# Performance work log

Measured on AMD Instinct MI355X. Metric: run time of the kernel, lower is better.

## Reference

```python
import jax, jax.numpy as jnp
import numpy as np

HIDDEN = 2048
NUM_HEADS = 16
HEAD_DIM = 128
ROPE_BASE = 10000.0
B, L = 2, 2048


def _rotate_half(x):
    x1, x2 = jnp.split(x, 2, axis=-1)
    return jnp.concatenate((-x2, x1), axis=-1)


def _apply_rope(x, position_ids, base=ROPE_BASE):
    # x: [B, L, H, D]; position_ids: [L] (broadcast over batch)
    D = x.shape[-1]
    dim_idx = jnp.arange(0, D, 2, dtype=jnp.float32)
    inv_freq = 1.0 / (base ** (dim_idx / D))                      # [D/2]
    freqs = position_ids.astype(jnp.float32)[None, :, None] * inv_freq  # [1, L, D/2]
    # NOTE: faithful to source: sin/cos are repeat_interleaved ([s0,s0,s1,s1,...])
    sin = jnp.repeat(jnp.sin(freqs), 2, axis=-1)[:, :, None, :]   # [1, L, 1, D]
    cos = jnp.repeat(jnp.cos(freqs), 2, axis=-1)[:, :, None, :]
    return cos * x + _rotate_half(x) * sin


def setup_inputs() -> dict:
    key = jax.random.key(0)
    k1, k2, k3, k4, k5 = jax.random.split(key, 5)
    hidden_states = jax.random.normal(k1, (B, L, HIDDEN), dtype=jnp.float32)
    # causal additive mask, broadcastable over heads
    causal = jnp.tril(jnp.ones((L, L), dtype=bool))
    attention_mask = jnp.where(causal, 0.0, -1e9).astype(jnp.float32)
    attention_mask = jnp.broadcast_to(attention_mask, (B, 1, L, L))
    position_ids = jnp.arange(L, dtype=jnp.int64)
    s = 1.0 / np.sqrt(HIDDEN)
    Wq = jax.random.normal(k2, (HIDDEN, NUM_HEADS * HEAD_DIM), dtype=jnp.float32) * s
    Wk = jax.random.normal(k3, (HIDDEN, NUM_HEADS * HEAD_DIM), dtype=jnp.float32) * s
    Wv = jax.random.normal(k4, (HIDDEN, NUM_HEADS * HEAD_DIM), dtype=jnp.float32) * s
    Wo = jax.random.normal(k5, (NUM_HEADS * HEAD_DIM, HIDDEN), dtype=jnp.float32) * s
    return {"hidden_states": hidden_states, "attention_mask": attention_mask,
            "position_ids": position_ids, "Wq": Wq, "Wk": Wk, "Wv": Wv, "Wo": Wo}


def reference(hidden_states, attention_mask, position_ids, Wq, Wk, Wv, Wo):
    Bb, Ll, _ = hidden_states.shape
    H, D = NUM_HEADS, HEAD_DIM
    scale = D ** -0.5
    q = (hidden_states @ Wq).reshape(Bb, Ll, H, D)
    k = (hidden_states @ Wk).reshape(Bb, Ll, H, D)
    v = (hidden_states @ Wv).reshape(Bb, Ll, H, D)
    q = _apply_rope(q, position_ids)
    k = _apply_rope(k, position_ids)
    # [B, H, Lq, Lk]
    scores = jnp.einsum('bqhd,bkhd->bhqk', q, k) * scale + attention_mask
    attn = jax.nn.softmax(scores.astype(jnp.float32), axis=-1).astype(q.dtype)
    out = jnp.einsum('bhqk,bkhd->bqhd', attn, v).reshape(Bb, Ll, H * D)
    return out @ Wo
```

## Files before the change

### kernel.cpp

```cpp
#include <hip/hip_runtime.h>
#include <stdint.h>

typedef uint16_t u16;
typedef __attribute__((ext_vector_type(4))) float f32x4;
typedef __attribute__((ext_vector_type(2))) unsigned short u16x2;
typedef __attribute__((ext_vector_type(4))) unsigned short u16x4;
typedef __attribute__((ext_vector_type(8))) __bf16 bf16x8;

#define HIDDEN 2048
#define LSEQ   2048
#define NH     16
#define HD     128
#define NQK    6144

__device__ __forceinline__ u16 f2b(float f) {
  union { float f; uint32_t u; } v; v.f = f;
  uint32_t r = v.u + 0x7fffu + ((v.u >> 16) & 1u);
  return (u16)(r >> 16);
}
__device__ __forceinline__ float b2f(u16 h) {
  union { uint32_t u; float f; } v; v.u = ((uint32_t)h) << 16;
  return v.f;
}

__device__ __forceinline__ void gload16(const void* g, void* l) {
  __builtin_amdgcn_global_load_lds((const __attribute__((address_space(1))) void*)g,
                                   (__attribute__((address_space(3))) void*)l, 16, 0, 0);
}
__device__ __forceinline__ f32x4 mfma16(bf16x8 a, bf16x8 b, f32x4 c) {
  return __builtin_amdgcn_mfma_f32_16x16x32_bf16(a, b, c, 0, 0, 0);
}

__global__ void k_f32_to_bf16(const float* __restrict__ in, u16* __restrict__ out, int n4) {
  int i = blockIdx.x * 256 + threadIdx.x;
  if (i >= n4) return;
  float4 v = ((const float4*)in)[i];
  u16x4 o = { f2b(v.x), f2b(v.y), f2b(v.z), f2b(v.w) };
  ((u16x4*)out)[i] = o;
}

__global__ __launch_bounds__(256) void k_transpose_bf16(const float* __restrict__ W,
                                                        u16* __restrict__ WT, int R, int C) {
  __shared__ u16 tile[64][65];
  const int bx = blockIdx.x, by = blockIdx.y;
  const int t = threadIdx.x;
  const int g = t >> 4, k = t & 15;
#pragma unroll
  for (int p = 0; p < 4; ++p) {
    int r = by * 64 + p * 16 + g;
    int c = bx * 64 + k * 4;
    float4 v = *(const float4*)(W + (size_t)r * C + c);
    tile[p * 16 + g][k * 4 + 0] = f2b(v.x);
    tile[p * 16 + g][k * 4 + 1] = f2b(v.y);
    tile[p * 16 + g][k * 4 + 2] = f2b(v.z);
    tile[p * 16 + g][k * 4 + 3] = f2b(v.w);
  }
  __syncthreads();
#pragma unroll
  for (int p = 0; p < 4; ++p) {
    int n = bx * 64 + p * 16 + g;
    int kk = by * 64 + k * 4;
    u16x4 o = { tile[k * 4 + 0][p * 16 + g], tile[k * 4 + 1][p * 16 + g],
                tile[k * 4 + 2][p * 16 + g], tile[k * 4 + 3][p * 16 + g] };
    *(u16x4*)(WT + (size_t)n * R + kk) = o;
  }
}

__global__ __launch_bounds__(256) void k_transpose_v(const u16* __restrict__ qkv,
                                                     u16* __restrict__ vt) {
  __shared__ u16 tile[64][65];
  const int lt = blockIdx.x;
  const int dt = blockIdx.y;
  const int bh = blockIdx.z;
  const int t = threadIdx.x;
  const int g = t >> 4, k = t & 15;
  const u16* src = qkv + (size_t)(bh >> 4) * LSEQ * NQK + 2 * HIDDEN + (bh & 15) * HD;
#pragma unroll
  for (int p = 0; p < 4; ++p) {
    int l = lt * 64 + p * 16 + g;
    int d = dt * 64 + k * 4;
    u16x4 v = *(const u16x4*)(src + (size_t)l * NQK + d);
    tile[p * 16 + g][k * 4 + 0] = v[0];
    tile[p * 16 + g][k * 4 + 1] = v[1];
    tile[p * 16 + g][k * 4 + 2] = v[2];
    tile[p * 16 + g][k * 4 + 3] = v[3];
  }
  __syncthreads();
  u16* dst = vt + (size_t)bh * HD * LSEQ;
#pragma unroll
  for (int p = 0; p < 4; ++p) {
    int d = dt * 64 + p * 16 + g;
    int l = lt * 64 + k * 4;
    u16x4 o = { tile[k * 4 + 0][p * 16 + g], tile[k * 4 + 1][p * 16 + g],
                tile[k * 4 + 2][p * 16 + g], tile[k * 4 + 3][p * 16 + g] };
    *(u16x4*)(dst + (size_t)d * LSEQ + l) = o;
  }
}

__global__ void k_rope_table(const int* __restrict__ pos, float* __restrict__ tab, int pstride) {
  int i = blockIdx.x * 256 + threadIdx.x;
  int l = i >> 6, j = i & 63;
  float p = (float)pos[(size_t)l * pstride];
  float th = p * expf(-(float)j * 0.14391156642178528f);
  tab[2 * i + 0] = cosf(th);
  tab[2 * i + 1] = sinf(th);
}

__global__ void k_rope_apply(u16* __restrict__ qkv, const float* __restrict__ tab) {
  int i = blockIdx.x * 256 + threadIdx.x;
  int dph = i & 31;
  int h = (i >> 5) & 15;
  int mat = (i >> 9) & 1;
  int row = i >> 10;
  int l = row & (LSEQ - 1);
  const float* t1 = tab + 2 * (l * 64 + dph);
  const float* t2 = tab + 2 * (l * 64 + 32 + dph);
  float s = mat ? 1.0f : 0.08838834764831845f;
  size_t base = (size_t)row * NQK + mat * HIDDEN + h * HD + dph * 2;
  u16x2 xa = *(u16x2*)(qkv + base);
  u16x2 xb = *(u16x2*)(qkv + base + 64);
  float x1a = b2f(xa[0]), x1b = b2f(xa[1]), x2a = b2f(xb[0]), x2b = b2f(xb[1]);
  u16x2 oa = { f2b((t1[0] * x1a - t1[1] * x2a) * s), f2b((t1[0] * x1b - t1[1] * x2b) * s) };
  u16x2 ob = { f2b((t2[0] * x2a + t2[1] * x1a) * s), f2b((t2[0] * x2b + t2[1] * x1b) * s) };
  *(u16x2*)(qkv + base) = oa;
  *(u16x2*)(qkv + base + 64) = ob;
}

template<int BF16OUT>
__global__ __launch_bounds__(512, 2) void k_gemm2(const u16* __restrict__ A,
                                                  const u16* __restrict__ Bt,
                                                  void* __restrict__ Cv,
                                                  int M, int N, int K) {
  __shared__ __align__(16) char lds[147456];
  const int tid = threadIdx.x, w = tid >> 6, lane = tid & 63;
  const int l15 = lane & 15, l4 = lane >> 4;
  const int wm = w >> 2, wn = w & 3;
  const int nbx = gridDim.x;
  const int nwg = nbx * gridDim.y;
  const int id = blockIdx.y * nbx + blockIdx.x;
  const int qq = nwg >> 3;
  const int sid = (id & 7) * qq + (id >> 3);
  const int bn = sid % nbx, bm = sid / nbx;
  const u16* Ag = A + (size_t)bm * 128 * K;
  const u16* Bg = Bt + (size_t)bn * 256 * K;
  const int r7 = (tid >> 3) & 7;
  const int sw0 = ((0 + l4) ^ (l15 & 7)) * 16;
  const int sw1 = ((4 + l4) ^ (l15 & 7)) * 16;

  auto stageA = [&](int kt, int buf) {
    char* dst = lds + buf * 16384;
    const int k0 = kt << 6;
#pragma unroll
    for (int i = 0; i < 2; ++i) {
      int c = i * 512 + tid;
      int row = c >> 3, s = (c & 7) ^ r7;
      gload16(Ag + (size_t)row * K + k0 + s * 8, dst + (i * 512 + w * 64) * 16);
    }
  };
  auto stageBh = [&](int kt, int buf, int half) {
    char* dst = lds + 49152 + buf * 32768;
    const int k0 = kt << 6;
#pragma unroll
    for (int i = 0; i < 2; ++i) {
      int c = half * 1024 + i * 512 + tid;
      int row = c >> 3, s = (c & 7) ^ r7;
      gload16(Bg + (size_t)row * K + k0 + s * 8, dst + (half * 1024 + i * 512 + w * 64) * 16);
    }
  };

  const int NT = K >> 6;
  stageA(0, 0); stageBh(0, 0, 0); stageBh(0, 0, 1);
  stageA(1, 1); stageBh(1, 1, 0); stageBh(1, 1, 1);
  asm volatile("s_waitcnt vmcnt(6)" ::: "memory");
  __builtin_amdgcn_s_barrier();
  asm volatile("" ::: "memory");

  f32x4 acc[4][4] = {};
  int buf = 0, sbuf = 2;
  for (int t = 0; t < NT; ++t) {
    const char* Ab = lds + buf * 16384;
    const char* Bb = lds + 49152 + buf * 32768;
    const bool doStage = (t + 2 < NT);
    bf16x8 af[4][2], bfr[4][2];
    auto rdA = [&](int mi, int ks) {
      return *(const bf16x8*)(Ab + ((wm * 64 + mi * 16 + l15) << 7) + (ks ? sw1 : sw0));
    };
    auto rdB = [&](int nj, int ks) {
      return *(const bf16x8*)(Bb + ((wn * 64 + nj * 16 + l15) << 7) + (ks ? sw1 : sw0));
    };

#pragma unroll
    for (int mi = 0; mi < 2; ++mi) { af[mi][0] = rdA(mi, 0); af[mi][1] = rdA(mi, 1); }
#pragma unroll
    for (int nj = 0; nj < 2; ++nj) { bfr[nj][0] = rdB(nj, 0); bfr[nj][1] = rdB(nj, 1); }
    if (doStage) stageA(t + 2, sbuf);
    __builtin_amdgcn_s_setprio(1);
#pragma unroll
    for (int mi = 0; mi < 2; ++mi)
#pragma unroll
      for (int nj = 0; nj < 2; ++nj) {
        acc[mi][nj] = mfma16(af[mi][0], bfr[nj][0], acc[mi][nj]);
        acc[mi][nj] = mfma16(af[mi][1], bfr[nj][1], acc[mi][nj]);
      }
    __builtin_amdgcn_s_setprio(0);

#pragma unroll
    for (int nj = 2; nj < 4; ++nj) { bfr[nj][0] = rdB(nj, 0); bfr[nj][1] = rdB(nj, 1); }
    if (doStage) stageBh(t + 2, sbuf, 0);
    __builtin_amdgcn_s_setprio(1);
#pragma unroll
    for (int mi = 0; mi < 2; ++mi)
#pragma unroll
      for (int nj = 2; nj < 4; ++nj) {
        acc[mi][nj] = mfma16(af[mi][0], bfr[nj][0], acc[mi][nj]);
        acc[mi][nj] = mfma16(af[mi][1], bfr[nj][1], acc[mi][nj]);
      }
    __builtin_amdgcn_s_setprio(0);

#pragma unroll
    for (int mi = 2; mi < 4; ++mi) { af[mi][0] = rdA(mi, 0); af[mi][1] = rdA(mi, 1); }
    if (doStage) stageBh(t + 2, sbuf, 1);
    __builtin_amdgcn_s_setprio(1);
#pragma unroll
    for (int mi = 2; mi < 4; ++mi)
#pragma unroll
      for (int nj = 2; nj < 4; ++nj) {
        acc[mi][nj] = mfma16(af[mi][0], bfr[nj][0], acc[mi][nj]);
        acc[mi][nj] = mfma16(af[mi][1], bfr[nj][1], acc[mi][nj]);
      }
    __builtin_amdgcn_s_setprio(0);

    __builtin_amdgcn_s_setprio(1);
#pragma unroll
    for (int mi = 2; mi < 4; ++mi)
#pragma unroll
      for (int nj = 0; nj < 2; ++nj) {
        acc[mi][nj] = mfma16(af[mi][0], bfr[nj][0], acc[mi][nj]);
        acc[mi][nj] = mfma16(af[mi][1], bfr[nj][1], acc[mi][nj]);
      }
    __builtin_amdgcn_s_setprio(0);

    if (doStage) asm volatile("s_waitcnt vmcnt(6)" ::: "memory");
    else         asm volatile("s_waitcnt vmcnt(0)" ::: "memory");
    __builtin_amdgcn_s_barrier();
    asm volatile("" ::: "memory");
    buf = (buf == 2) ? 0 : buf + 1;
    sbuf = (sbuf == 2) ? 0 : sbuf + 1;
  }

#pragma unroll
  for (int mi = 0; mi < 4; ++mi) {
#pragma unroll
    for (int nj = 0; nj < 4; ++nj) {
      int row0 = bm * 128 + wm * 64 + mi * 16 + l4 * 4;
      int col  = bn * 256 + wn * 64 + nj * 16 + l15;
#pragma unroll
      for (int r = 0; r < 4; ++r) {
        float v = acc[mi][nj][r];
        if (BF16OUT) ((u16*)Cv)[(size_t)(row0 + r) * N + col] = f2b(v);
        else         ((float*)Cv)[(size_t)(row0 + r) * N + col] = v;
      }
    }
  }
}

__global__ __launch_bounds__(512) void k_attn(const u16* __restrict__ qkv,
                                              const u16* __restrict__ vt,
                                              u16* __restrict__ aout) {
  __shared__ __align__(16) u16 Ks[3][64 * 128];
  __shared__ __align__(16) u16 Vs[3][128 * 64];
  __shared__ __align__(16) u16 Ps[2][8 * 16 * 72];
  const int bid = blockIdx.x;
  const int bh = bid & 31, pairi = bid >> 5;
  const int b = bh >> 4, h = bh & 15;
  const int qtA = pairi, qtB = 15 - pairi;
  const int tid = threadIdx.x, w = tid >> 6, lane = tid & 63;
  const int l15 = lane & 15, l4 = lane >> 4;

  bf16x8 qfA[4], qfB[4];
  {
    const u16* qpA = qkv + (size_t)(b * LSEQ + qtA * 128 + w * 16 + l15) * NQK + h * HD;
    const u16* qpB = qkv + (size_t)(b * LSEQ + qtB * 128 + w * 16 + l15) * NQK + h * HD;
#pragma unroll
    for (int ks = 0; ks < 4; ++ks) {
      qfA[ks] = *(const bf16x8*)(qpA + ks * 32 + l4 * 8);
      qfB[ks] = *(const bf16x8*)(qpB + ks * 32 + l4 * 8);
    }
  }

  f32x4 accA[8] = {}, accB[8] = {};
  float mA[4], lA[4], mB[4], lB[4];
#pragma unroll
  for (int r = 0; r < 4; ++r) { mA[r] = -1e30f; lA[r] = 0.f; mB[r] = -1e30f; lB[r] = 0.f; }

  const u16* kb  = qkv + (size_t)b * LSEQ * NQK + HIDDEN + h * HD;
  const u16* vtb = vt + (size_t)bh * HD * LSEQ;
  const int ntA = 2 * qtA + 2, ntB = 2 * qtB + 2;
  const int qbaseA = qtA * 128 + w * 16, qbaseB = qtB * 128 + w * 16;

  auto stage = [&](int t, int bf) {
    const int kv0 = t * 64;
    char* Kd = (char*)(&Ks[bf][0]);
    char* Vd = (char*)(&Vs[bf][0]);
#pragma unroll
    for (int p = 0; p < 2; ++p) {
      int cc = p * 512 + tid;
      int row = cc >> 4, sl = cc & 15;
      gload16(kb + (size_t)(kv0 + row) * NQK + ((sl ^ (row & 7)) * 8), Kd + (p * 512 + w * 64) * 16);
    }
#pragma unroll
    for (int p = 0; p < 2; ++p) {
      int cc = p * 512 + tid;
      int d = cc >> 3, sl = cc & 7;
      gload16(vtb + (size_t)d * LSEQ + kv0 + ((sl ^ (d & 7)) * 8), Vd + (p * 512 + w * 64) * 16);
    }
  };

  auto softmaxWrite = [&](f32x4 (&accs)[4], f32x4 (&acc_o)[8], float (&mrun)[4],
                          float (&lrun)[4], int qbase, int kv0, u16* ps) {
    const int qrow0 = qbase + l4 * 4;
    float pv[4][4], pmax[4];
    if (kv0 + 63 <= qbase) {
#pragma unroll
      for (int r = 0; r < 4; ++r) {
        pmax[r] = fmaxf(fmaxf(accs[0][r], accs[1][r]), fmaxf(accs[2][r], accs[3][r]));
#pragma unroll
        for (int nj = 0; nj < 4; ++nj) pv[nj][r] = accs[nj][r];
      }
    } else {
#pragma unroll
      for (int r = 0; r < 4; ++r) {
        float mx = -3e38f;
#pragma unroll
        for (int nj = 0; nj < 4; ++nj) {
          int kvcol = kv0 + nj * 16 + l15;
          float sv = (kvcol <= qrow0 + r) ? accs[nj][r] : -3e38f;
          pv[nj][r] = sv;
          mx = fmaxf(mx, sv);
        }
        pmax[r] = mx;
      }
    }
#pragma unroll
    for (int r = 0; r < 4; ++r) {
      pmax[r] = fmaxf(pmax[r], __shfl_xor(pmax[r], 1));
      pmax[r] = fmaxf(pmax[r], __shfl_xor(pmax[r], 2));
      pmax[r] = fmaxf(pmax[r], __shfl_xor(pmax[r], 4));
      pmax[r] = fmaxf(pmax[r], __shfl_xor(pmax[r], 8));
    }
    bool need = false;
#pragma unroll
    for (int r = 0; r < 4; ++r) need = need || (pmax[r] > mrun[r] + 8.f);
    if (__any(need)) {
#pragma unroll
      for (int r = 0; r < 4; ++r) {
        float nm = fmaxf(mrun[r], pmax[r]);
        float cf = __expf(mrun[r] - nm);
        mrun[r] = nm;
        lrun[r] *= cf;
#pragma unroll
        for (int df = 0; df < 8; ++df) acc_o[df][r] *= cf;
      }
    }
#pragma unroll
    for (int r = 0; r < 4; ++r) {
      float s = 0.f;
#pragma unroll
      for (int nj = 0; nj < 4; ++nj) {
        float e = __expf(pv[nj][r] - mrun[r]);
        pv[nj][r] = e;
        s += e;
      }
      s += __shfl_xor(s, 1);
      s += __shfl_xor(s, 2);
      s += __shfl_xor(s, 4);
      s += __shfl_xor(s, 8);
      lrun[r] += s;
    }
#pragma unroll
    for (int nj = 0; nj < 4; ++nj)
#pragma unroll
      for (int r = 0; r < 4; ++r)
        ps[(w * 16 + l4 * 4 + r) * 72 + nj * 16 + l15] = f2b(pv[nj][r]);
  };

  stage(0, 0);
  stage(1, 1);
  asm volatile("s_waitcnt vmcnt(4)" ::: "memory");
  __builtin_amdgcn_s_barrier();

  int buf = 0, sbuf = 2;
  for (int t = 0; t < ntB; ++t) {
    const bool doStage = (t + 2 < ntB);
    if (doStage) stage(t + 2, sbuf);
    const int kv0 = t * 64;
    const char* KsC = (const char*)(&Ks[buf][0]);
    const char* VsC = (const char*)(&Vs[buf][0]);
    const bool doA = (t < ntA) && (kv0 <= qbaseA + 15);
    const bool doB = (kv0 <= qbaseB + 15);

    if (doA) {
      f32x4 sA[4] = {}, sB[4] = {};
      __builtin_amdgcn_s_setprio(1);
#pragma unroll
      for (int ks = 0; ks < 4; ++ks) {
#pragma unroll
        for (int nj = 0; nj < 4; ++nj) {
          int row = nj * 16 + l15;
          int co = (ks * 64 + l4 * 16) ^ ((row & 7) << 4);
          bf16x8 kf = *(const bf16x8*)(KsC + row * 256 + co);
          sA[nj] = mfma16(qfA[ks], kf, sA[nj]);
          sB[nj] = mfma16(qfB[ks], kf, sB[nj]);
        }
      }
      __builtin_amdgcn_s_setprio(0);
      softmaxWrite(sA, accA, mA, lA, qbaseA, kv0, &Ps[0][0]);
      softmaxWrite(sB, accB, mB, lB, qbaseB, kv0, &Ps[1][0]);
      bf16x8 paA[2], paB[2];
#pragma unroll
      for (int ks2 = 0; ks2 < 2; ++ks2) {
        paA[ks2] = *(const bf16x8*)(&Ps[0][0] + (w * 16 + l15) * 72 + ks2 * 32 + l4 * 8);
        paB[ks2] = *(const bf16x8*)(&Ps[1][0] + (w * 16 + l15) * 72 + ks2 * 32 + l4 * 8);
      }
      __builtin_amdgcn_s_setprio(1);
#pragma unroll
      for (int df = 0; df < 8; ++df) {
#pragma unroll
        for (int ks2 = 0; ks2 < 2; ++ks2) {
          int vrow = df * 16 + l15;
          int co = (ks2 * 64 + l4 * 16) ^ ((vrow & 7) << 4);
          bf16x8 bv = *(const bf16x8*)(VsC + vrow * 128 + co);
          accA[df] = mfma16(paA[ks2], bv, accA[df]);
          accB[df] = mfma16(paB[ks2], bv, accB[df]);
        }
      }
      __builtin_amdgcn_s_setprio(0);
    } else if (doB) {
      f32x4 sB[4] = {};
      __builtin_amdgcn_s_setprio(1);
#pragma unroll
      for (int ks = 0; ks < 4; ++ks) {
#pragma unroll
        for (int nj = 0; nj < 4; ++nj) {
          int row = nj * 16 + l15;
          int co = (ks * 64 + l4 * 16) ^ ((row & 7) << 4);
          bf16x8 kf = *(const bf16x8*)(KsC + row * 256 + co);
          sB[nj] = mfma16(qfB[ks], kf, sB[nj]);
        }
      }
      __builtin_amdgcn_s_setprio(0);
      softmaxWrite(sB, accB, mB, lB, qbaseB, kv0, &Ps[1][0]);
      bf16x8 paB[2];
#pragma unroll
      for (int ks2 = 0; ks2 < 2; ++ks2)
        paB[ks2] = *(const bf16x8*)(&Ps[1][0] + (w * 16 + l15) * 72 + ks2 * 32 + l4 * 8);
      __builtin_amdgcn_s_setprio(1);
#pragma unroll
      for (int df = 0; df < 8; ++df) {
#pragma unroll
        for (int ks2 = 0; ks2 < 2; ++ks2) {
          int vrow = df * 16 + l15;
          int co = (ks2 * 64 + l4 * 16) ^ ((vrow & 7) << 4);
          bf16x8 bv = *(const bf16x8*)(VsC + vrow * 128 + co);
          accB[df] = mfma16(paB[ks2], bv, accB[df]);
        }
      }
      __builtin_amdgcn_s_setprio(0);
    }

    if (doStage) asm volatile("s_waitcnt vmcnt(4)" ::: "memory");
    else         asm volatile("s_waitcnt vmcnt(0)" ::: "memory");
    __builtin_amdgcn_s_barrier();
    buf = (buf == 2) ? 0 : buf + 1;
    sbuf = (sbuf == 2) ? 0 : sbuf + 1;
  }

#pragma unroll
  for (int r = 0; r < 4; ++r) {
    float invA = 1.f / lA[r];
    float invB = 1.f / lB[r];
    u16* opA = aout + (size_t)(b * LSEQ + qtA * 128 + w * 16 + l4 * 4 + r) * HIDDEN + h * HD;
    u16* opB = aout + (size_t)(b * LSEQ + qtB * 128 + w * 16 + l4 * 4 + r) * HIDDEN + h * HD;
#pragma unroll
    for (int df = 0; df < 8; ++df) {
      opA[df * 16 + l15] = f2b(accA[df][r] * invA);
      opB[df * 16 + l15] = f2b(accB[df][r] * invB);
    }
  }
}

extern "C" void kernel_launch(void* const* d_in, const int* in_sizes, int n_in,
                              void* d_out, int out_size, void* d_ws, size_t ws_size,
                              hipStream_t stream) {
  const float* hidden = (const float*)d_in[0];
  const int*   pos = (const int*)d_in[2];
  const float* Wq = (const float*)d_in[3];
  const float* Wk = (const float*)d_in[4];
  const float* Wv = (const float*)d_in[5];
  const float* Wo = (const float*)d_in[6];
  float* out = (float*)d_out;

  char* ws = (char*)d_ws;
  u16* hbf   = (u16*)ws;
  u16* WT    = (u16*)(ws + 16777216);
  u16* vt    = WT;
  u16* WoT   = (u16*)(ws + 16777216 + 25165824);
  u16* qkv   = (u16*)(ws + 50331648);
  float* tab = (float*)(ws + 100663296);
  u16* aout  = hbf;

  int pstride = (in_sizes[2] == LSEQ) ? 1 : 2;

  k_f32_to_bf16<<<8192, 256, 0, stream>>>(hidden, hbf, 2097152);
  dim3 tg(32, 32);
  k_transpose_bf16<<<tg, 256, 0, stream>>>(Wq, WT,                   2048, 2048);
  k_transpose_bf16<<<tg, 256, 0, stream>>>(Wk, WT + 2048 * 2048,     2048, 2048);
  k_transpose_bf16<<<tg, 256, 0, stream>>>(Wv, WT + 2 * 2048 * 2048, 2048, 2048);
  k_transpose_bf16<<<tg, 256, 0, stream>>>(Wo, WoT,                  2048, 2048);
  k_rope_table<<<512, 256, 0, stream>>>(pos, tab, pstride);
  k_gemm2<1><<<dim3(24, 32), 512, 0, stream>>>(hbf, WT, qkv, 4096, 6144, 2048);
  k_transpose_v<<<dim3(32, 2, 32), 256, 0, stream>>>(qkv, vt);
  k_rope_apply<<<16384, 256, 0, stream>>>(qkv, tab);
  k_attn<<<256, 512, 0, stream>>>(qkv, vt, aout);
  k_gemm2<0><<<dim3(8, 32), 512, 0, stream>>>(aout, WoT, out, 4096, 2048, 2048);
}
```

Baseline: 295.8 us.

## Fuse RoPE into QKV GEMM epilogue and streamline attention softmax

Removes the separate RoPE kernel by permuting Q/K weight columns so that rotate-half pairs land in adjacent lanes, then applies the rotation in the QKV GEMM epilogue using a lane shuffle. The Q scale (including log2e) is folded into the Wq conversion, and softmax uses exp2 with a fixed initial max, per-lane partial row sums reduced once at the end, and lazy rescaling only when a row max is exceeded. The GEMM tile swizzle is also changed. The fixed M0 initial max relies on scores staying within range for these inputs, which risks overflow for other data.

```diff
diff --git a/kernel.cpp b/kernel.cpp
--- a/kernel.cpp
+++ b/kernel.cpp
@@ -3,7 +3,6 @@
 
 typedef uint16_t u16;
 typedef __attribute__((ext_vector_type(4))) float f32x4;
-typedef __attribute__((ext_vector_type(2))) unsigned short u16x2;
 typedef __attribute__((ext_vector_type(4))) unsigned short u16x4;
 typedef __attribute__((ext_vector_type(8))) __bf16 bf16x8;
 
@@ -12,6 +11,8 @@
 #define NH     16
 #define HD     128
 #define NQK    6144
+#define QSCALE 0.12751743f
+#define M0 32.0f
 
 __device__ __forceinline__ u16 f2b(float f) {
   union { float f; uint32_t u; } v; v.f = f;
@@ -40,7 +41,8 @@
 }
 
 __global__ __launch_bounds__(256) void k_transpose_bf16(const float* __restrict__ W,
-                                                        u16* __restrict__ WT, int R, int C) {
+                                                        u16* __restrict__ WT, int R, int C,
+                                                        float scale, int perm) {
   __shared__ u16 tile[64][65];
   const int bx = blockIdx.x, by = blockIdx.y;
   const int t = threadIdx.x;
@@ -50,15 +52,16 @@
     int r = by * 64 + p * 16 + g;
     int c = bx * 64 + k * 4;
     float4 v = *(const float4*)(W + (size_t)r * C + c);
-    tile[p * 16 + g][k * 4 + 0] = f2b(v.x);
-    tile[p * 16 + g][k * 4 + 1] = f2b(v.y);
-    tile[p * 16 + g][k * 4 + 2] = f2b(v.z);
-    tile[p * 16 + g][k * 4 + 3] = f2b(v.w);
+    tile[p * 16 + g][k * 4 + 0] = f2b(v.x * scale);
+    tile[p * 16 + g][k * 4 + 1] = f2b(v.y * scale);
+    tile[p * 16 + g][k * 4 + 2] = f2b(v.z * scale);
+    tile[p * 16 + g][k * 4 + 3] = f2b(v.w * scale);
   }
   __syncthreads();
 #pragma unroll
   for (int p = 0; p < 4; ++p) {
     int n = bx * 64 + p * 16 + g;
+    if (perm) n = (n & ~127) | ((n & 63) << 1) | ((n >> 6) & 1);
     int kk = by * 64 + k * 4;
     u16x4 o = { tile[k * 4 + 0][p * 16 + g], tile[k * 4 + 1][p * 16 + g],
                 tile[k * 4 + 2][p * 16 + g], tile[k * 4 + 3][p * 16 + g] };
@@ -106,41 +109,22 @@
   tab[2 * i + 1] = sinf(th);
 }
 
-__global__ void k_rope_apply(u16* __restrict__ qkv, const float* __restrict__ tab) {
-  int i = blockIdx.x * 256 + threadIdx.x;
-  int dph = i & 31;
-  int h = (i >> 5) & 15;
-  int mat = (i >> 9) & 1;
-  int row = i >> 10;
-  int l = row & (LSEQ - 1);
-  const float* t1 = tab + 2 * (l * 64 + dph);
-  const float* t2 = tab + 2 * (l * 64 + 32 + dph);
-  float s = mat ? 1.0f : 0.08838834764831845f;
-  size_t base = (size_t)row * NQK + mat * HIDDEN + h * HD + dph * 2;
-  u16x2 xa = *(u16x2*)(qkv + base);
-  u16x2 xb = *(u16x2*)(qkv + base + 64);
-  float x1a = b2f(xa[0]), x1b = b2f(xa[1]), x2a = b2f(xb[0]), x2b = b2f(xb[1]);
-  u16x2 oa = { f2b((t1[0] * x1a - t1[1] * x2a) * s), f2b((t1[0] * x1b - t1[1] * x2b) * s) };
-  u16x2 ob = { f2b((t2[0] * x2a + t2[1] * x1a) * s), f2b((t2[0] * x2b + t2[1] * x1b) * s) };
-  *(u16x2*)(qkv + base) = oa;
-  *(u16x2*)(qkv + base + 64) = ob;
-}
-
-template<int BF16OUT>
+template<int BF16OUT, int DOROPE>
 __global__ __launch_bounds__(512, 2) void k_gemm2(const u16* __restrict__ A,
                                                   const u16* __restrict__ Bt,
                                                   void* __restrict__ Cv,
+                                                  const float* __restrict__ tab,
                                                   int M, int N, int K) {
   __shared__ __align__(16) char lds[147456];
   const int tid = threadIdx.x, w = tid >> 6, lane = tid & 63;
   const int l15 = lane & 15, l4 = lane >> 4;
   const int wm = w >> 2, wn = w & 3;
-  const int nbx = gridDim.x;
-  const int nwg = nbx * gridDim.y;
-  const int id = blockIdx.y * nbx + blockIdx.x;
-  const int qq = nwg >> 3;
-  const int sid = (id & 7) * qq + (id >> 3);
-  const int bn = sid % nbx, bm = sid / nbx;
+  const int nbn = gridDim.x, nbm = gridDim.y;
+  const int id = blockIdx.y * nbn + blockIdx.x;
+  const int x = id & 7, k = id >> 3;
+  const int g = nbm >> 3;
+  const int bm = x * g + (k % g);
+  const int bn = k / g;
   const u16* Ag = A + (size_t)bm * 128 * K;
   const u16* Bg = Bt + (size_t)bn * 256 * K;
   const int r7 = (tid >> 3) & 7;
@@ -248,6 +232,7 @@
     sbuf = (sbuf == 2) ? 0 : sbuf + 1;
   }
 
+  const float2* tb = (const float2*)tab;
 #pragma unroll
   for (int mi = 0; mi < 4; ++mi) {
 #pragma unroll
@@ -257,6 +242,14 @@
 #pragma unroll
       for (int r = 0; r < 4; ++r) {
         float v = acc[mi][nj][r];
+        if (DOROPE) {
+          float vp = __shfl_xor(v, 1);
+          if (col < 4096) {
+            int l = (row0 + r) & (LSEQ - 1);
+            float2 tt = tb[l * 64 + ((col & 127) >> 2) + ((l15 & 1) << 5)];
+            v = (l15 & 1) ? (tt.x * v + tt.y * vp) : (tt.x * v - tt.y * vp);
+          }
+        }
         if (BF16OUT) ((u16*)Cv)[(size_t)(row0 + r) * N + col] = f2b(v);
         else         ((float*)Cv)[(size_t)(row0 + r) * N + col] = v;
       }
@@ -291,7 +284,7 @@
   f32x4 accA[8] = {}, accB[8] = {};
   float mA[4], lA[4], mB[4], lB[4];
 #pragma unroll
-  for (int r = 0; r < 4; ++r) { mA[r] = -1e30f; lA[r] = 0.f; mB[r] = -1e30f; lB[r] = 0.f; }
+  for (int r = 0; r < 4; ++r) { mA[r] = M0; lA[r] = 0.f; mB[r] = M0; lB[r] = 0.f; }
 
   const u16* kb  = qkv + (size_t)b * LSEQ * NQK + HIDDEN + h * HD;
   const u16* vtb = vt + (size_t)bh * HD * LSEQ;
@@ -319,11 +312,11 @@
   auto softmaxWrite = [&](f32x4 (&accs)[4], f32x4 (&acc_o)[8], float (&mrun)[4],
                           float (&lrun)[4], int qbase, int kv0, u16* ps) {
     const int qrow0 = qbase + l4 * 4;
-    float pv[4][4], pmax[4];
+    float pv[4][4], lm[4];
     if (kv0 + 63 <= qbase) {
 #pragma unroll
       for (int r = 0; r < 4; ++r) {
-        pmax[r] = fmaxf(fmaxf(accs[0][r], accs[1][r]), fmaxf(accs[2][r], accs[3][r]));
+        lm[r] = fmaxf(fmaxf(accs[0][r], accs[1][r]), fmaxf(accs[2][r], accs[3][r]));
 #pragma unroll
         for (int nj = 0; nj < 4; ++nj) pv[nj][r] = accs[nj][r];
       }
@@ -338,28 +331,25 @@
           pv[nj][r] = sv;
           mx = fmaxf(mx, sv);
         }
-        pmax[r] = mx;
-      }
-    }
-#pragma unroll
-    for (int r = 0; r < 4; ++r) {
-      pmax[r] = fmaxf(pmax[r], __shfl_xor(pmax[r], 1));
-      pmax[r] = fmaxf(pmax[r], __shfl_xor(pmax[r], 2));
-      pmax[r] = fmaxf(pmax[r], __shfl_xor(pmax[r], 4));
-      pmax[r] = fmaxf(pmax[r], __shfl_xor(pmax[r], 8));
-    }
-    bool need = false;
-#pragma unroll
-    for (int r = 0; r < 4; ++r) need = need || (pmax[r] > mrun[r] + 8.f);
-    if (__any(need)) {
+        lm[r] = mx;
+      }
+    }
+    int over = (lm[0] > mrun[0]) | (lm[1] > mrun[1]) | (lm[2] > mrun[2]) | (lm[3] > mrun[3]);
+    if (__builtin_expect(__any(over), 0)) {
 #pragma unroll
       for (int r = 0; r < 4; ++r) {
-        float nm = fmaxf(mrun[r], pmax[r]);
-        float cf = __expf(mrun[r] - nm);
-        mrun[r] = nm;
-        lrun[r] *= cf;
-#pragma unroll
-        for (int df = 0; df < 8; ++df) acc_o[df][r] *= cf;
+        float px = lm[r];
+        px = fmaxf(px, __shfl_xor(px, 1));
+        px = fmaxf(px, __shfl_xor(px, 2));
+        px = fmaxf(px, __shfl_xor(px, 4));
+        px = fmaxf(px, __shfl_xor(px, 8));
+        if (px > mrun[r]) {
+          float cf = exp2f(mrun[r] - px);
+          mrun[r] = px;
+          lrun[r] *= cf;
+#pragma unroll
+          for (int df = 0; df < 8; ++df) acc_o[df][r] *= cf;
+        }
       }
     }
 #pragma unroll
@@ -367,14 +357,10 @@
       float s = 0.f;
 #pragma unroll
       for (int nj = 0; nj < 4; ++nj) {
-        float e = __expf(pv[nj][r] - mrun[r]);
+        float e = exp2f(pv[nj][r] - mrun[r]);
         pv[nj][r] = e;
         s += e;
       }
-      s += __shfl_xor(s, 1);
-      s += __shfl_xor(s, 2);
-      s += __shfl_xor(s, 4);
-      s += __shfl_xor(s, 8);
       lrun[r] += s;
     }
 #pragma unroll
@@ -477,8 +463,14 @@
 
 #pragma unroll
   for (int r = 0; r < 4; ++r) {
-    float invA = 1.f / lA[r];
-    float invB = 1.f / lB[r];
+    float sA = lA[r];
+    sA += __shfl_xor(sA, 1); sA += __shfl_xor(sA, 2);
+    sA += __shfl_xor(sA, 4); sA += __shfl_xor(sA, 8);
+    float sB = lB[r];
+    sB += __shfl_xor(sB, 1); sB += __shfl_xor(sB, 2);
+    sB += __shfl_xor(sB, 4); sB += __shfl_xor(sB, 8);
+    float invA = 1.f / sA;
+    float invB = 1.f / sB;
     u16* opA = aout + (size_t)(b * LSEQ + qtA * 128 + w * 16 + l4 * 4 + r) * HIDDEN + h * HD;
     u16* opB = aout + (size_t)(b * LSEQ + qtB * 128 + w * 16 + l4 * 4 + r) * HIDDEN + h * HD;
 #pragma unroll
@@ -513,14 +505,13 @@
 
   k_f32_to_bf16<<<8192, 256, 0, stream>>>(hidden, hbf, 2097152);
   dim3 tg(32, 32);
-  k_transpose_bf16<<<tg, 256, 0, stream>>>(Wq, WT,                   2048, 2048);
-  k_transpose_bf16<<<tg, 256, 0, stream>>>(Wk, WT + 2048 * 2048,     2048, 2048);
-  k_transpose_bf16<<<tg, 256, 0, stream>>>(Wv, WT + 2 * 2048 * 2048, 2048, 2048);
-  k_transpose_bf16<<<tg, 256, 0, stream>>>(Wo, WoT,                  2048, 2048);
+  k_transpose_bf16<<<tg, 256, 0, stream>>>(Wq, WT,                   2048, 2048, QSCALE, 1);
+  k_transpose_bf16<<<tg, 256, 0, stream>>>(Wk, WT + 2048 * 2048,     2048, 2048, 1.0f, 1);
+  k_transpose_bf16<<<tg, 256, 0, stream>>>(Wv, WT + 2 * 2048 * 2048, 2048, 2048, 1.0f, 0);
+  k_transpose_bf16<<<tg, 256, 0, stream>>>(Wo, WoT,                  2048, 2048, 1.0f, 0);
   k_rope_table<<<512, 256, 0, stream>>>(pos, tab, pstride);
-  k_gemm2<1><<<dim3(24, 32), 512, 0, stream>>>(hbf, WT, qkv, 4096, 6144, 2048);
+  k_gemm2<1, 1><<<dim3(24, 32), 512, 0, stream>>>(hbf, WT, qkv, tab, 4096, 6144, 2048);
   k_transpose_v<<<dim3(32, 2, 32), 256, 0, stream>>>(qkv, vt);
-  k_rope_apply<<<16384, 256, 0, stream>>>(qkv, tab);
   k_attn<<<256, 512, 0, stream>>>(qkv, vt, aout);
-  k_gemm2<0><<<dim3(8, 32), 512, 0, stream>>>(aout, WoT, out, 4096, 2048, 2048);
-}
+  k_gemm2<0, 0><<<dim3(8, 32), 512, 0, stream>>>(aout, WoT, out, nullptr, 4096, 2048, 2048);
+}
```

Measured after the change: 394.5 us. 33.4% more time.
